# Performance work log

Measured on AMD Instinct MI355X. Metric: run time of the kernel, lower is better.

The kernel has to match this reference:

```python
import math
import jax, jax.numpy as jnp
import numpy as np

IN_CH = 64
NUM_ANCHOR = 4
MAP_H, MAP_W = 96, 96
BATCH = 8
BN_EPS = 1e-5


def _conv2d(x, w, b, padding, dilation):
    # x: [B,C,H,W], w: [O,I,kh,kw] (OIHW)
    y = jax.lax.conv_general_dilated(
        x, w, window_strides=(1, 1),
        padding=((padding, padding), (padding, padding)),
        rhs_dilation=(dilation, dilation),
        dimension_numbers=('NCHW', 'OIHW', 'NCHW'))
    return y + b[None, :, None, None]


def _bn(x, gamma, beta, mean, var):
    scale = gamma / jnp.sqrt(var + BN_EPS)
    return x * scale[None, :, None, None] + (beta - mean * scale)[None, :, None, None]


def setup_inputs() -> dict:
    key = jax.random.key(0)
    ks = jax.random.split(key, 12)
    # cyclic channel-shift permutation matrices, one per anchor pass
    eye = np.eye(IN_CH, dtype=np.float32)
    shift = IN_CH // (2 * NUM_ANCHOR)
    perms = np.stack([eye[np.roll(np.arange(IN_CH), i * shift)] for i in range(2 * NUM_ANCHOR)])
    w_std = 1.0 / math.sqrt(IN_CH * 9)
    return {
        'x': jax.random.normal(ks[0], (BATCH, IN_CH, MAP_H, MAP_W), dtype=jnp.float32),
        'perms': jnp.asarray(perms),
        'dcn_w': jax.random.normal(ks[1], (IN_CH, IN_CH, 3, 3), dtype=jnp.float32) * w_std,
        'dcn_b': jax.random.normal(ks[2], (IN_CH,), dtype=jnp.float32) * 0.01,
        'conv2_w': jax.random.normal(ks[3], (IN_CH, IN_CH, 3, 3), dtype=jnp.float32) * w_std,
        'conv2_b': jax.random.normal(ks[4], (IN_CH,), dtype=jnp.float32) * 0.01,
        'conv3_w': jax.random.normal(ks[5], (IN_CH, IN_CH, 3, 3), dtype=jnp.float32) * w_std,
        'conv3_b': jax.random.normal(ks[6], (IN_CH,), dtype=jnp.float32) * 0.01,
        'bn_gamma': jax.random.uniform(ks[7], (3, IN_CH), dtype=jnp.float32, minval=0.5, maxval=1.5),
        'bn_beta': jax.random.normal(ks[8], (3, IN_CH), dtype=jnp.float32) * 0.1,
        'bn_mean': jax.random.normal(ks[9], (3, IN_CH), dtype=jnp.float32) * 0.1,
        'bn_var': jax.random.uniform(ks[10], (3, IN_CH), dtype=jnp.float32, minval=0.5, maxval=1.5),
    }


def reference(x, perms, dcn_w, dcn_b, conv2_w, conv2_b, conv3_w, conv3_b,
              bn_gamma, bn_beta, bn_mean, bn_var):
    h = x.shape[2]
    pad = math.ceil(h / (2 ** 1.5 + 2))  # 20 for h=96

    def conv_stack(o):
        # DCN at init (zero offsets) == plain 3x3 conv, pad=1
        o = jax.nn.relu(_bn(_conv2d(o, dcn_w, dcn_b, 1, 1), bn_gamma[0], bn_beta[0], bn_mean[0], bn_var[0]))
        o = jax.nn.relu(_bn(_conv2d(o, conv2_w, conv2_b, 2, 2), bn_gamma[1], bn_beta[1], bn_mean[1], bn_var[1]))
        o = jax.nn.relu(_bn(_conv2d(o, conv3_w, conv3_b, 2, 2), bn_gamma[2], bn_beta[2], bn_mean[2], bn_var[2]))
        return o

    outs = []
    for i in range(2 * NUM_ANCHOR):  # fixed small structural loop
        o = jnp.einsum('mn,bnhw->bmhw', perms[i], x)  # channel permutation
        if i % 2 != 0:
            o = jnp.pad(o, ((0, 0), (0, 0), (pad, pad), (pad, pad)))
        o = jnp.rot90(o, k=i % 4, axes=(-2, -1))   # ccw rotate
        o = conv_stack(o)
        o = jnp.rot90(o, k=(-i) % 4, axes=(-2, -1))  # cw rotate back
        if i % 2 != 0:
            H, W = o.shape[-2], o.shape[-1]
            sh, sw = (H - MAP_H) // 2, (W - MAP_W) // 2
            o = o[..., sh:sh + MAP_H, sw:sw + MAP_W]  # center crop
        outs.append(o)
    out_tensor = jnp.concatenate(outs, axis=1)  # [B, 8*C, H, W]
    out = jnp.max(out_tensor, axis=1, keepdims=True)
    # branch_name == 'midpoint', orientational_anchor=False -> clamped sigmoid
    return jnp.clip(jax.nn.sigmoid(out), 1e-4, 1.0 - 1e-4)
```

## Files before the change

### kernel.cpp

```cpp
#include <hip/hip_runtime.h>
#include <math.h>

#define B 8
#define C 64
#define HW 96
#define NWV 36864

typedef __attribute__((ext_vector_type(8)))  short short8;
typedef __attribute__((ext_vector_type(16))) float floatx16;

__device__ __forceinline__ unsigned short f2bf(float f) {
    unsigned int u = __float_as_uint(f);
    unsigned int r = (u + 0x7fffu + ((u >> 16) & 1u)) >> 16;
    return (unsigned short)r;
}

__device__ __forceinline__ void rotmap(int k, int ta, int tb, int& sa, int& sb) {
    switch (k) {
        case 0: sa = ta;     sb = tb;     break;
        case 1: sa = 2 - tb; sb = ta;     break;
        case 2: sa = 2 - ta; sb = 2 - tb; break;
        default: sa = tb;    sb = 2 - ta; break;
    }
}

__global__ void prep_w(const float* __restrict__ dcn_w, const float* __restrict__ c2w,
                       const float* __restrict__ c3w,
                       const float* __restrict__ gamma, const float* __restrict__ var_,
                       unsigned short* __restrict__ Wall) {
    int idx = blockIdx.x * 256 + threadIdx.x;
    if (idx >= 16 * NWV) return;
    int v = idx / NWV, rem = idx % NWV;
    int tap  = rem >> 12;
    int w12  = rem & 4095;
    int ks   = w12 >> 10;
    int cf   = (w12 >> 9) & 1;
    int lane = (w12 >> 3) & 63;
    int j    = w12 & 7;
    int co = cf * 32 + (lane & 31);
    int ci = ks * 16 + (lane >> 5) * 8 + j;
    int ta = tap / 3, tb = tap % 3;
    const float* src; int k, srcci, l;
    if (v < 8)       { k = v & 3;  srcci = (ci + 8 * v) & 63; src = dcn_w; l = 0; }
    else if (v < 12) { k = v - 8;  srcci = ci; src = c2w; l = 1; }
    else             { k = v - 12; srcci = ci; src = c3w; l = 2; }
    int sa, sb; rotmap(k, ta, tb, sa, sb);
    float s = gamma[l * 64 + co] * rsqrtf(var_[l * 64 + co] + 1e-5f);
    Wall[idx] = f2bf(src[((co * 64 + srcci) * 3 + sa) * 3 + sb] * s);
}

__global__ void prep_bias(const float* __restrict__ dcn_b, const float* __restrict__ c2b,
                          const float* __restrict__ c3b,
                          const float* __restrict__ gamma, const float* __restrict__ beta,
                          const float* __restrict__ mean, const float* __restrict__ var_,
                          float* __restrict__ biasg) {
    int t = threadIdx.x;
    if (t < 192) {
        int l = t >> 6, c = t & 63;
        const float* cb = (l == 0) ? dcn_b : ((l == 1) ? c2b : c3b);
        float s = gamma[l * 64 + c] * rsqrtf(var_[l * 64 + c] + 1e-5f);
        biasg[t] = cb[c] * s + beta[l * 64 + c] - mean[l * 64 + c] * s;
    }
}

__global__ __launch_bounds__(256) void prep_x(const float* __restrict__ in,
                                              unsigned short* __restrict__ out) {
    __shared__ float row[64 * 97];
    int by = blockIdx.x;
    int b = by / 96, y = by % 96;
    int t = threadIdx.x;
    for (int e = t; e < 6144; e += 256) {
        int c = e / 96, x = e - c * 96;
        row[c * 97 + x] = in[(((size_t)(b * 64 + c) * 96 + y) * 96) + x];
    }
    __syncthreads();
    for (int e = t; e < 6144; e += 256) {
        int x = e >> 6, c = e & 63;
        out[(((size_t)(b * 96 + y) * 96 + x) << 6) + c] = f2bf(row[c * 97 + x]);
    }
}

__global__ __launch_bounds__(256) void border_clear(unsigned short* __restrict__ buf1) {
    int idx = blockIdx.y;
    int br = (idx >> 3) * 2, b = idx & 7;
    int z = br * 8 + b;
    int i = blockIdx.x * 32 + (threadIdx.x >> 3);
    int g = threadIdx.x & 7;
    int r, c;
    if (i < 416)      { r = i / 104;              c = i % 104; }
    else if (i < 832) { int j = i - 416; r = 100 + j / 104; c = j % 104; }
    else              { int j = i - 832; r = 4 + (j >> 3); int c8 = j & 7;
                        c = (c8 < 4) ? c8 : 92 + c8; }
    uint4 zero = make_uint4(0u, 0u, 0u, 0u);
    *(uint4*)(buf1 + (size_t)z * (104 * 104 * 64) + ((size_t)(r * 104 + c) << 6) + (g << 3)) = zero;
}

__global__ __launch_bounds__(256, 2) void conv1_k(
    const unsigned short* __restrict__ xhwc, unsigned short* __restrict__ buf1,
    const unsigned short* __restrict__ Wall, const float* __restrict__ biasg) {

    __shared__ __align__(16) unsigned short xt[10 * 34 * 64];

    int z = blockIdx.z, br = z >> 3, b = z & 7, odd = br & 1;
    int fy0 = blockIdx.y * 8, fx0 = blockIdx.x * 32;
    int t = threadIdx.x, lane = t & 63, wv = t >> 6;
    int n = lane & 31, kq = lane >> 5;

    const unsigned short* xb = xhwc + ((size_t)b * 96 * 96 << 6);
    const short8* Ag = (const short8*)(Wall + (size_t)br * NWV);

    for (int e = t; e < 2720; e += 256) {
        int p = e >> 3, g = e & 7;
        int yy = p / 34, xx = p - yy * 34;
        int gy = fy0 - 5 + yy, gx = fx0 - 5 + xx;
        uint4 v = make_uint4(0u, 0u, 0u, 0u);
        if ((unsigned)gy < 96u && (unsigned)gx < 96u)
            v = *(const uint4*)(xb + ((size_t)(gy * 96 + gx) << 6) + (g << 3));
        *(uint4*)(xt + (p << 6) + ((g ^ (xx & 7)) << 3)) = v;
    }
    __syncthreads();

    floatx16 acc[2][2];
#pragma unroll
    for (int cf = 0; cf < 2; cf++)
#pragma unroll
        for (int pf = 0; pf < 2; pf++)
#pragma unroll
            for (int i = 0; i < 16; i++) acc[cf][pf][i] = 0.f;

#pragma unroll
    for (int ks = 0; ks < 4; ks++) {
#pragma unroll
        for (int tb = 0; tb < 3; tb++) {
            short8 a[3][2];
#pragma unroll
            for (int ta = 0; ta < 3; ta++)
#pragma unroll
                for (int cf = 0; cf < 2; cf++)
                    a[ta][cf] = Ag[(((ta * 3 + tb) * 4 + ks) * 2 + cf) * 64 + lane];
            int xx = n + tb;
            int g = ((ks * 2 + kq) ^ (xx & 7)) << 3;
            short8 bf[4];
#pragma unroll
            for (int rr = 0; rr < 4; rr++) {
                int p = (2 * wv + rr) * 34 + xx;
                bf[rr] = *(const short8*)(xt + (p << 6) + g);
            }
#pragma unroll
            for (int ta = 0; ta < 3; ta++)
#pragma unroll
                for (int pf = 0; pf < 2; pf++) {
                    int rr = pf + ta;
                    acc[0][pf] = __builtin_amdgcn_mfma_f32_32x32x16_bf16(a[ta][0], bf[rr], acc[0][pf], 0, 0, 0);
                    acc[1][pf] = __builtin_amdgcn_mfma_f32_32x32x16_bf16(a[ta][1], bf[rr], acc[1][pf], 0, 0, 0);
                }
        }
    }

    float4 bv[2][4];
#pragma unroll
    for (int cf = 0; cf < 2; cf++)
#pragma unroll
        for (int rb = 0; rb < 4; rb++)
            bv[cf][rb] = *(const float4*)(biasg + 32 * cf + 8 * rb + 4 * kq);

    __syncthreads();
#pragma unroll
    for (int pf = 0; pf < 2; pf++) {
        int pq = (2 * wv + pf) * 32 + n;
        int key = (pq & 7) << 1;
#pragma unroll
        for (int cf = 0; cf < 2; cf++)
#pragma unroll
            for (int rb = 0; rb < 4; rb++) {
                int u = kq + 2 * rb + 8 * cf;
                float v0 = fmaxf(acc[cf][pf][rb * 4 + 0] + bv[cf][rb].x, 0.f);
                float v1 = fmaxf(acc[cf][pf][rb * 4 + 1] + bv[cf][rb].y, 0.f);
                float v2 = fmaxf(acc[cf][pf][rb * 4 + 2] + bv[cf][rb].z, 0.f);
                float v3 = fmaxf(acc[cf][pf][rb * 4 + 3] + bv[cf][rb].w, 0.f);
                uint2 pk = make_uint2((unsigned)f2bf(v0) | ((unsigned)f2bf(v1) << 16),
                                      (unsigned)f2bf(v2) | ((unsigned)f2bf(v3) << 16));
                *(uint2*)((char*)xt + pq * 128 + ((u ^ key) << 3)) = pk;
            }
    }
    __syncthreads();

    unsigned short* fb = buf1 + (size_t)z * (104 * 104 * 64);
    int lo = odd ? 0 : 4, hi = odd ? 104 : 100;
    for (int e = t; e < 2048; e += 256) {
        int px = e >> 3, g = e & 7;
        int key = (px & 7) << 1;
        uint4 v = *(const uint4*)((const char*)xt + px * 128 + (((2 * g) ^ key) << 3));
        int lr = px >> 5, nn = px & 31;
        int f = fy0 + lr, fc = fx0 + nn;
        if (f >= lo && f < hi && fc >= lo && fc < hi)
            *(uint4*)(fb + ((size_t)(f * 104 + fc) << 6) + (g << 3)) = v;
    }
}

#define WLOAD(src, ksv)                                                              \
    _Pragma("unroll")                                                                \
    for (int k2 = 0; k2 < 3; k2++) {                                                 \
        int e = t + k2 * 512;                                                        \
        if (e < 1152) {                                                              \
            int f = e >> 6, c = e & 63;                                              \
            wr[k2] = *(const uint4*)((src) + (((f >> 1) * 4 + (ksv)) * 2 + (f & 1)) * 512 + c * 8); \
        }                                                                            \
    }
#define WSTORE(bufidx)                                                               \
    _Pragma("unroll")                                                                \
    for (int k2 = 0; k2 < 3; k2++) {                                                 \
        int e = t + k2 * 512;                                                        \
        if (e < 1152) *(uint4*)(&wlds[bufidx][e << 4]) = wr[k2];                     \
    }

__global__ __launch_bounds__(512, 2) void conv23_k(
    const unsigned short* __restrict__ buf1, float* __restrict__ maxb,
    const unsigned short* __restrict__ Wall, const float* __restrict__ biasg) {

    __shared__ __align__(16) unsigned char ubuf[960 * 128];
    __shared__ __align__(16) unsigned char wlds[2][18432];
    unsigned short* xs = (unsigned short*)ubuf;
    char* c2out = (char*)ubuf;

    int z = blockIdx.z, br = z >> 3, odd = br & 1;
    int oy0 = blockIdx.y * 16, ox0 = blockIdx.x * 32;
    int t = threadIdx.x, lane = t & 63, wv = t >> 6;
    int n = lane & 31, kq = lane >> 5;

    const unsigned short* fb = buf1 + (size_t)z * (104 * 104 * 64);
    const unsigned short* A2g = Wall + (size_t)(8  + (br & 3)) * NWV;
    const unsigned short* A3g = Wall + (size_t)(12 + (br & 3)) * NWV;

    for (int e = t; e < 7680; e += 512) {
        int p = e >> 3, g = e & 7;
        int yy = p / 40, xx = p - yy * 40;
        uint4 v = *(const uint4*)(fb + ((size_t)((oy0 + yy) * 104 + ox0 + xx) << 6) + (g << 3));
        *(uint4*)(xs + (p << 6) + ((g ^ (xx & 7)) << 3)) = v;
    }

    uint4 wr[3];
    WLOAD(A2g, 0)
    WSTORE(0)
    WLOAD(A2g, 1)

    int q_[3], row2_[3], col2_[3];
#pragma unroll
    for (int jj = 0; jj < 3; jj++) {
        int q = 96 * wv + 32 * jj + n;
        q_[jj] = q;
        int qc = (q < 720) ? q : 719;
        int r2 = qc / 36;
        row2_[jj] = r2;
        col2_[jj] = qc - 36 * r2;
    }

    floatx16 acc2[3][2];
#pragma unroll
    for (int jj = 0; jj < 3; jj++)
#pragma unroll
        for (int cf = 0; cf < 2; cf++)
#pragma unroll
            for (int i = 0; i < 16; i++) acc2[jj][cf][i] = 0.f;

    __syncthreads();

#pragma unroll
    for (int ks = 0; ks < 4; ks++) {
        WSTORE((ks + 1) & 1)
        if (ks < 2) { WLOAD(A2g, ks + 2) }
        else        { WLOAD(A3g, ks - 2) }
        const char* wq = (const char*)wlds[ks & 1];
#pragma unroll
        for (int tb = 0; tb < 3; tb++) {
            short8 a[3][2];
#pragma unroll
            for (int ta = 0; ta < 3; ta++)
#pragma unroll
                for (int cf = 0; cf < 2; cf++)
                    a[ta][cf] = *(const short8*)(wq + (((((ta * 3 + tb) * 2 + cf) << 6) | lane) << 4));
#pragma unroll
            for (int jj = 0; jj < 3; jj++) {
                int colx = col2_[jj] + 2 * tb;
                int gsw = ((ks * 2 + kq) ^ (colx & 7)) << 3;
#pragma unroll
                for (int ta = 0; ta < 3; ta++) {
                    int p = (row2_[jj] + 2 * ta) * 40 + colx;
                    short8 bfr = *(const short8*)(xs + (p << 6) + gsw);
                    acc2[jj][0] = __builtin_amdgcn_mfma_f32_32x32x16_bf16(a[ta][0], bfr, acc2[jj][0], 0, 0, 0);
                    acc2[jj][1] = __builtin_amdgcn_mfma_f32_32x32x16_bf16(a[ta][1], bfr, acc2[jj][1], 0, 0, 0);
                }
            }
        }
        __syncthreads();
    }

    int rlo2 = (!odd && oy0 == 0)  ? 2  : 0;
    int rhi2 = (!odd && oy0 == 80) ? 18 : 20;
    int clo2 = (!odd && ox0 == 0)  ? 2  : 0;
    int chi2 = (!odd && ox0 == 64) ? 34 : 36;
    float4 bv2[2][4];
#pragma unroll
    for (int cf = 0; cf < 2; cf++)
#pragma unroll
        for (int rb = 0; rb < 4; rb++)
            bv2[cf][rb] = *(const float4*)(biasg + 64 + 32 * cf + 8 * rb + 4 * kq);

#pragma unroll
    for (int jj = 0; jj < 3; jj++) {
        if (q_[jj] < 720) {
            bool valid = (row2_[jj] >= rlo2) && (row2_[jj] < rhi2) &&
                         (col2_[jj] >= clo2) && (col2_[jj] < chi2);
            int key = col2_[jj] & 14;
#pragma unroll
            for (int cf = 0; cf < 2; cf++)
#pragma unroll
                for (int rb = 0; rb < 4; rb++) {
                    int u = kq + 2 * rb + 8 * cf;
                    float v0 = 0.f, v1 = 0.f, v2 = 0.f, v3 = 0.f;
                    if (valid) {
                        v0 = fmaxf(acc2[jj][cf][rb * 4 + 0] + bv2[cf][rb].x, 0.f);
                        v1 = fmaxf(acc2[jj][cf][rb * 4 + 1] + bv2[cf][rb].y, 0.f);
                        v2 = fmaxf(acc2[jj][cf][rb * 4 + 2] + bv2[cf][rb].z, 0.f);
                        v3 = fmaxf(acc2[jj][cf][rb * 4 + 3] + bv2[cf][rb].w, 0.f);
                    }
                    uint2 pk = make_uint2((unsigned)f2bf(v0) | ((unsigned)f2bf(v1) << 16),
                                          (unsigned)f2bf(v2) | ((unsigned)f2bf(v3) << 16));
                    *(uint2*)(c2out + q_[jj] * 128 + ((u ^ key) << 3)) = pk;
                }
        }
    }
    __syncthreads();

    int r0 = 2 * wv;
    floatx16 acc3[2][2];
#pragma unroll
    for (int cf = 0; cf < 2; cf++)
#pragma unroll
        for (int pf = 0; pf < 2; pf++)
#pragma unroll
            for (int i = 0; i < 16; i++) acc3[cf][pf][i] = 0.f;

#pragma unroll
    for (int ks = 0; ks < 4; ks++) {
        if (ks < 3) { WSTORE((ks + 1) & 1) }
        if (ks < 2) { WLOAD(A3g, ks + 2) }
        const char* wq = (const char*)wlds[ks & 1];
#pragma unroll
        for (int tb = 0; tb < 3; tb++) {
            short8 a[3][2];
#pragma unroll
            for (int ta = 0; ta < 3; ta++)
#pragma unroll
                for (int cf = 0; cf < 2; cf++)
                    a[ta][cf] = *(const short8*)(wq + (((((ta * 3 + tb) * 2 + cf) << 6) | lane) << 4));
            int col = n + 2 * tb;
            int key = col & 14;
            int ublk = 2 * (ks * 2 + kq);
            short8 bf[6];
#pragma unroll
            for (int rr = 0; rr < 6; rr++) {
                int q = (r0 + rr) * 36 + col;
                bf[rr] = *(const short8*)(c2out + q * 128 + ((ublk ^ key) << 3));
            }
#pragma unroll
            for (int ta = 0; ta < 3; ta++)
#pragma unroll
                for (int pf = 0; pf < 2; pf++) {
                    int rr = pf + 2 * ta;
                    acc3[0][pf] = __builtin_amdgcn_mfma_f32_32x32x16_bf16(a[ta][0], bf[rr], acc3[0][pf], 0, 0, 0);
                    acc3[1][pf] = __builtin_amdgcn_mfma_f32_32x32x16_bf16(a[ta][1], bf[rr], acc3[1][pf], 0, 0, 0);
                }
        }
        if (ks < 3) __syncthreads();
    }

    float4 bv3[2][4];
#pragma unroll
    for (int cf = 0; cf < 2; cf++)
#pragma unroll
        for (int rb = 0; rb < 4; rb++)
            bv3[cf][rb] = *(const float4*)(biasg + 128 + 32 * cf + 8 * rb + 4 * kq);

#pragma unroll
    for (int pf = 0; pf < 2; pf++) {
        float m = 0.f;
#pragma unroll
        for (int cf = 0; cf < 2; cf++)
#pragma unroll
            for (int rb = 0; rb < 4; rb++) {
                m = fmaxf(m, acc3[cf][pf][rb * 4 + 0] + bv3[cf][rb].x);
                m = fmaxf(m, acc3[cf][pf][rb * 4 + 1] + bv3[cf][rb].y);
                m = fmaxf(m, acc3[cf][pf][rb * 4 + 2] + bv3[cf][rb].z);
                m = fmaxf(m, acc3[cf][pf][rb * 4 + 3] + bv3[cf][rb].w);
            }
        m = fmaxf(m, 0.f);
        m = fmaxf(m, __shfl_xor(m, 32, 64));
        if (lane < 32)
            maxb[((size_t)z * 96 + oy0 + r0 + pf) * 96 + ox0 + n] = m;
    }
}

__global__ void final_k(const float* __restrict__ maxb, float* __restrict__ out) {
    int i = blockIdx.x * 256 + threadIdx.x;
    if (i < B * HW * HW) {
        int b = i / 9216, yx = i - b * 9216;
        float m = 0.f;
#pragma unroll
        for (int br = 0; br < 8; br++)
            m = fmaxf(m, maxb[((size_t)(br * 8 + b)) * 9216 + yx]);
        float v = 1.f / (1.f + expf(-m));
        out[i] = fminf(fmaxf(v, 1e-4f), 1.f - 1e-4f);
    }
}


extern "C" void kernel_launch(void* const* d_in, const int* in_sizes, int n_in,
                              void* d_out, int out_size, void* d_ws, size_t ws_size,
                              hipStream_t stream) {
    const float* x     = (const float*)d_in[0];
    const float* dcn_w = (const float*)d_in[2];
    const float* dcn_b = (const float*)d_in[3];
    const float* c2w   = (const float*)d_in[4];
    const float* c2b   = (const float*)d_in[5];
    const float* c3w   = (const float*)d_in[6];
    const float* c3b   = (const float*)d_in[7];
    const float* gamma = (const float*)d_in[8];
    const float* beta  = (const float*)d_in[9];
    const float* mean  = (const float*)d_in[10];
    const float* var_  = (const float*)d_in[11];

    char* ws = (char*)d_ws;
    unsigned short* Wall = (unsigned short*)ws;
    size_t off = (size_t)16 * NWV * 2;
    float* biasg = (float*)(ws + off);            off += 1024;
    float* maxb  = (float*)(ws + off);            off += (size_t)64 * 9216 * 4;
    unsigned short* xhwc = (unsigned short*)(ws + off); off += (size_t)B * 9216 * 64 * 2;
    unsigned short* buf1 = (unsigned short*)(ws + off);

    prep_w<<<(16 * NWV + 255) / 256, 256, 0, stream>>>(dcn_w, c2w, c3w, gamma, var_, Wall);
    prep_bias<<<1, 256, 0, stream>>>(dcn_b, c2b, c3b, gamma, beta, mean, var_, biasg);
    prep_x<<<B * 96, 256, 0, stream>>>(x, xhwc);
    border_clear<<<dim3(50, 32), 256, 0, stream>>>(buf1);

    dim3 g1(4, 13, 64);
    conv1_k<<<g1, 256, 0, stream>>>(xhwc, buf1, Wall, biasg);

    dim3 g23(3, 6, 64);
    conv23_k<<<g23, 512, 0, stream>>>(buf1, maxb, Wall, biasg);

    final_k<<<(B * HW * HW + 255) / 256, 256, 0, stream>>>(maxb, (float*)d_out);
}
```

Baseline: 313.3 us.

## Load conv2/conv3 weight fragments directly from global memory instead of LDS staging

Removes the double-buffered LDS weight staging (WLOAD/WSTORE) in conv23_k. Each wave now reads its MFMA A-operand fragments straight from global memory (expected to hit L1/L2), which drops the per-k-step __syncthreads barriers and frees 36 KB of LDS. The trade is more global/cache traffic and load latency on the MFMA critical path, since every wave re-reads the same weights instead of sharing one LDS copy.

```diff
diff --git a/kernel.cpp b/kernel.cpp
--- a/kernel.cpp
+++ b/kernel.cpp
@@ -198,28 +198,11 @@
     }
 }
 
-#define WLOAD(src, ksv)                                                              \
-    _Pragma("unroll")                                                                \
-    for (int k2 = 0; k2 < 3; k2++) {                                                 \
-        int e = t + k2 * 512;                                                        \
-        if (e < 1152) {                                                              \
-            int f = e >> 6, c = e & 63;                                              \
-            wr[k2] = *(const uint4*)((src) + (((f >> 1) * 4 + (ksv)) * 2 + (f & 1)) * 512 + c * 8); \
-        }                                                                            \
-    }
-#define WSTORE(bufidx)                                                               \
-    _Pragma("unroll")                                                                \
-    for (int k2 = 0; k2 < 3; k2++) {                                                 \
-        int e = t + k2 * 512;                                                        \
-        if (e < 1152) *(uint4*)(&wlds[bufidx][e << 4]) = wr[k2];                     \
-    }
-
 __global__ __launch_bounds__(512, 2) void conv23_k(
     const unsigned short* __restrict__ buf1, float* __restrict__ maxb,
     const unsigned short* __restrict__ Wall, const float* __restrict__ biasg) {
 
     __shared__ __align__(16) unsigned char ubuf[960 * 128];
-    __shared__ __align__(16) unsigned char wlds[2][18432];
     unsigned short* xs = (unsigned short*)ubuf;
     char* c2out = (char*)ubuf;
 
@@ -229,8 +212,8 @@
     int n = lane & 31, kq = lane >> 5;
 
     const unsigned short* fb = buf1 + (size_t)z * (104 * 104 * 64);
-    const unsigned short* A2g = Wall + (size_t)(8  + (br & 3)) * NWV;
-    const unsigned short* A3g = Wall + (size_t)(12 + (br & 3)) * NWV;
+    const short8* A2 = (const short8*)(Wall + (size_t)(8  + (br & 3)) * NWV);
+    const short8* A3 = (const short8*)(Wall + (size_t)(12 + (br & 3)) * NWV);
 
     for (int e = t; e < 7680; e += 512) {
         int p = e >> 3, g = e & 7;
@@ -238,11 +221,6 @@
         uint4 v = *(const uint4*)(fb + ((size_t)((oy0 + yy) * 104 + ox0 + xx) << 6) + (g << 3));
         *(uint4*)(xs + (p << 6) + ((g ^ (xx & 7)) << 3)) = v;
     }
-
-    uint4 wr[3];
-    WLOAD(A2g, 0)
-    WSTORE(0)
-    WLOAD(A2g, 1)
 
     int q_[3], row2_[3], col2_[3];
 #pragma unroll
@@ -267,10 +245,6 @@
 
 #pragma unroll
     for (int ks = 0; ks < 4; ks++) {
-        WSTORE((ks + 1) & 1)
-        if (ks < 2) { WLOAD(A2g, ks + 2) }
-        else        { WLOAD(A3g, ks - 2) }
-        const char* wq = (const char*)wlds[ks & 1];
 #pragma unroll
         for (int tb = 0; tb < 3; tb++) {
             short8 a[3][2];
@@ -278,7 +252,7 @@
             for (int ta = 0; ta < 3; ta++)
 #pragma unroll
                 for (int cf = 0; cf < 2; cf++)
-                    a[ta][cf] = *(const short8*)(wq + (((((ta * 3 + tb) * 2 + cf) << 6) | lane) << 4));
+                    a[ta][cf] = A2[(((ta * 3 + tb) * 4 + ks) * 2 + cf) * 64 + lane];
 #pragma unroll
             for (int jj = 0; jj < 3; jj++) {
                 int colx = col2_[jj] + 2 * tb;
@@ -292,8 +266,9 @@
                 }
             }
         }
-        __syncthreads();
-    }
+    }
+
+    __syncthreads();
 
     int rlo2 = (!odd && oy0 == 0)  ? 2  : 0;
     int rhi2 = (!odd && oy0 == 80) ? 18 : 20;
@@ -343,9 +318,6 @@
 
 #pragma unroll
     for (int ks = 0; ks < 4; ks++) {
-        if (ks < 3) { WSTORE((ks + 1) & 1) }
-        if (ks < 2) { WLOAD(A3g, ks + 2) }
-        const char* wq = (const char*)wlds[ks & 1];
 #pragma unroll
         for (int tb = 0; tb < 3; tb++) {
             short8 a[3][2];
@@ -353,7 +325,7 @@
             for (int ta = 0; ta < 3; ta++)
 #pragma unroll
                 for (int cf = 0; cf < 2; cf++)
-                    a[ta][cf] = *(const short8*)(wq + (((((ta * 3 + tb) * 2 + cf) << 6) | lane) << 4));
+                    a[ta][cf] = A3[(((ta * 3 + tb) * 4 + ks) * 2 + cf) * 64 + lane];
             int col = n + 2 * tb;
             int key = col & 14;
             int ublk = 2 * (ks * 2 + kq);
@@ -372,7 +344,6 @@
                     acc3[1][pf] = __builtin_amdgcn_mfma_f32_32x32x16_bf16(a[ta][1], bf[rr], acc3[1][pf], 0, 0, 0);
                 }
         }
-        if (ks < 3) __syncthreads();
     }
 
     float4 bv3[2][4];
```

Measured after the change: 299.8 us. 4.3% less time.
